# Kernel tuning notes

Hardware: AMD Instinct MI355X
Metric: run time of the kernel (lower is better)

Reference implementation:

```python
import jax, jax.numpy as jnp
import numpy as np

N_NODES = 100000
N_EDGES = 3200000
N_FEAT = 512
N_HID = 16
N_CLS = 7


def setup_inputs() -> dict:
    key = jax.random.key(0)
    k0, k1, k2, k3 = jax.random.split(key, 4)
    x = jax.random.normal(k0, (N_NODES, N_FEAT), dtype=jnp.float32)
    edge_index = jax.random.randint(k1, (2, N_EDGES), 0, N_NODES, dtype=jnp.int64)
    W1 = jax.random.normal(k2, (N_FEAT, N_HID), dtype=jnp.float32) * (1.0 / np.sqrt(N_FEAT))
    b1 = jnp.zeros((N_HID,), dtype=jnp.float32)
    W2 = jax.random.normal(k3, (N_HID, N_CLS), dtype=jnp.float32) * (1.0 / np.sqrt(N_HID))
    b2 = jnp.zeros((N_CLS,), dtype=jnp.float32)
    return {"x": x, "edge_index": edge_index, "W1": W1, "b1": b1, "W2": W2, "b2": b2}


def _graph_conv(x, src, dst, W, b, n_nodes):
    # transform-then-aggregate: keeps the gathered edge tensor at hidden width
    h = x @ W                                      # [N, out]
    agg = jax.ops.segment_sum(h[src], dst, num_segments=n_nodes)  # [N, out]
    return agg + b


def reference(x, edge_index, W1, b1, W2, b2):
    src, dst = edge_index[0], edge_index[1]
    h = jax.nn.relu(_graph_conv(x, src, dst, W1, b1, N_NODES))
    # dropout is identity in eval mode
    out = _graph_conv(h, src, dst, W2, b2, N_NODES)
    return jax.nn.log_softmax(out, axis=1)
```

## Files before the change

kernel.cpp:

```cpp
#include <hip/hip_runtime.h>

#define NN 100000
#define NE 3200000
#define NF 512
#define NH 16
#define NC 7

__global__ __launch_bounds__(256) void gemm1_kernel(const float* __restrict__ x,
                                                    const float* __restrict__ W1,
                                                    float* __restrict__ h0) {
  const int lane = threadIdx.x & 63;
  const int wave = (blockIdx.x * blockDim.x + threadIdx.x) >> 6;
  const int nwaves = (gridDim.x * blockDim.x) >> 6;

  float w[8][NH];
#pragma unroll
  for (int i = 0; i < 4; ++i) {
#pragma unroll
    for (int j = 0; j < NH; ++j) {
      w[i][j]     = W1[(4 * lane + i) * NH + j];
      w[4 + i][j] = W1[(256 + 4 * lane + i) * NH + j];
    }
  }

  for (int row = wave; row < NN; row += nwaves) {
    const float4* xr = (const float4*)(x + (size_t)row * NF);
    float4 a0 = xr[lane];
    float4 a1 = xr[64 + lane];
    float a[8] = {a0.x, a0.y, a0.z, a0.w, a1.x, a1.y, a1.z, a1.w};

    float acc[NH];
#pragma unroll
    for (int j = 0; j < NH; ++j) acc[j] = 0.f;
#pragma unroll
    for (int i = 0; i < 8; ++i) {
#pragma unroll
      for (int j = 0; j < NH; ++j) acc[j] += a[i] * w[i][j];
    }

    float outv = 0.f;
#pragma unroll
    for (int j = 0; j < NH; ++j) {
      float v = acc[j];
      v += __shfl_xor(v, 1);
      v += __shfl_xor(v, 2);
      v += __shfl_xor(v, 4);
      v += __shfl_xor(v, 8);
      v += __shfl_xor(v, 16);
      v += __shfl_xor(v, 32);
      if (lane == j) outv = v;
    }
    if (lane < NH) h0[(size_t)row * NH + lane] = outv;
  }
}

__global__ __launch_bounds__(256) void scatter16_kernel(const int* __restrict__ ei,
                                                        const float* __restrict__ h0,
                                                        float* __restrict__ agg) {
  long long gid = (long long)blockIdx.x * blockDim.x + threadIdx.x;
  int e = (int)(gid >> 4);
  if (e >= NE) return;
  int j = (int)(gid & 15);
  int s = ei[e];
  int d = ei[NE + e];
  atomicAdd(&agg[(size_t)d * NH + j], h0[(size_t)s * NH + j]);
}

__global__ __launch_bounds__(256) void transform_kernel(const float* __restrict__ agg1,
                                                        const float* __restrict__ b1,
                                                        const float* __restrict__ W2,
                                                        float* __restrict__ p) {
  int n = blockIdx.x * blockDim.x + threadIdx.x;
  if (n >= NN) return;
  const float4* r = (const float4*)(agg1 + (size_t)n * NH);
  float4 v0 = r[0], v1 = r[1], v2 = r[2], v3 = r[3];
  float h[NH] = {v0.x, v0.y, v0.z, v0.w, v1.x, v1.y, v1.z, v1.w,
                 v2.x, v2.y, v2.z, v2.w, v3.x, v3.y, v3.z, v3.w};
#pragma unroll
  for (int k = 0; k < NH; ++k) h[k] = fmaxf(h[k] + b1[k], 0.f);

#pragma unroll
  for (int j = 0; j < NC; ++j) {
    float acc = 0.f;
#pragma unroll
    for (int k = 0; k < NH; ++k) acc += h[k] * W2[k * NC + j];
    p[(size_t)n * 8 + j] = acc;
  }
}

__global__ __launch_bounds__(256) void scatter7_kernel(const int* __restrict__ ei,
                                                       const float* __restrict__ p,
                                                       float* __restrict__ agg) {
  long long gid = (long long)blockIdx.x * blockDim.x + threadIdx.x;
  int e = (int)(gid >> 3);
  if (e >= NE) return;
  int j = (int)(gid & 7);
  if (j >= NC) return;
  int s = ei[e];
  int d = ei[NE + e];
  atomicAdd(&agg[(size_t)d * 8 + j], p[(size_t)s * 8 + j]);
}

__global__ __launch_bounds__(256) void lsm_kernel(const float* __restrict__ agg2,
                                                  const float* __restrict__ b2,
                                                  float* __restrict__ out) {
  int n = blockIdx.x * blockDim.x + threadIdx.x;
  if (n >= NN) return;
  float z[NC];
  float m = -1e30f;
#pragma unroll
  for (int j = 0; j < NC; ++j) {
    z[j] = agg2[(size_t)n * 8 + j] + b2[j];
    m = fmaxf(m, z[j]);
  }
  float s = 0.f;
#pragma unroll
  for (int j = 0; j < NC; ++j) s += __expf(z[j] - m);
  float l = __logf(s);
#pragma unroll
  for (int j = 0; j < NC; ++j) out[(size_t)n * NC + j] = z[j] - m - l;
}

extern "C" void kernel_launch(void* const* d_in, const int* in_sizes, int n_in,
                              void* d_out, int out_size, void* d_ws, size_t ws_size,
                              hipStream_t stream) {
  const float* x  = (const float*)d_in[0];
  const int*   ei = (const int*)d_in[1];
  const float* W1 = (const float*)d_in[2];
  const float* b1 = (const float*)d_in[3];
  const float* W2 = (const float*)d_in[4];
  const float* b2 = (const float*)d_in[5];
  float* out = (float*)d_out;

  float* bufA = (float*)d_ws;
  float* bufB = bufA + (size_t)NN * NH;

  hipMemsetAsync(bufB, 0, (size_t)NN * NH * sizeof(float), stream);
  gemm1_kernel<<<2048, 256, 0, stream>>>(x, W1, bufA);
  scatter16_kernel<<<(int)(((long long)NE * 16 + 255) / 256), 256, 0, stream>>>(ei, bufA, bufB);
  transform_kernel<<<(NN + 255) / 256, 256, 0, stream>>>(bufB, b1, W2, bufA);
  hipMemsetAsync(bufB, 0, (size_t)NN * 8 * sizeof(float), stream);
  scatter7_kernel<<<(int)(((long long)NE * 8 + 255) / 256), 256, 0, stream>>>(ei, bufA, bufB);
  lsm_kernel<<<(NN + 255) / 256, 256, 0, stream>>>(bufB, b2, out);
}
```

Baseline: 704.9 us.

## Bucket edges by destination and aggregate in shared memory with fused epilogues

Edges are partitioned into buckets of 128 destination nodes using a histogram, a scan and a partition pass. Each agg kernel then accumulates one bucket in LDS, which replaces global float atomics, and fuses the bias/ReLU/W2 transform and the log-softmax into its epilogue. The GEMM now processes two rows per wave and uses a butterfly transpose-reduce instead of 16 separate full reductions. Sorting costs extra passes over the edge list plus a packed edge buffer, and the packing relies on node ids fitting in 17 bits.

```diff
diff --git a/kernel.cpp b/kernel.cpp
--- a/kernel.cpp
+++ b/kernel.cpp
@@ -6,119 +6,244 @@
 #define NH 16
 #define NC 7
 
+#define NBUCK 782
+#define PBLK 196
+#define EPT 64
+
+__device__ __forceinline__ float reduce16(const float acc[16], int lane) {
+  float w8[8];
+#pragma unroll
+  for (int i = 0; i < 8; ++i) {
+    float sel = (lane & 1) ? acc[2 * i + 1] : acc[2 * i];
+    float oth = (lane & 1) ? acc[2 * i]     : acc[2 * i + 1];
+    w8[i] = sel + __shfl_xor(oth, 1);
+  }
+  float w4[4];
+#pragma unroll
+  for (int i = 0; i < 4; ++i) {
+    float sel = (lane & 2) ? w8[2 * i + 1] : w8[2 * i];
+    float oth = (lane & 2) ? w8[2 * i]     : w8[2 * i + 1];
+    w4[i] = sel + __shfl_xor(oth, 2);
+  }
+  float w2[2];
+#pragma unroll
+  for (int i = 0; i < 2; ++i) {
+    float sel = (lane & 4) ? w4[2 * i + 1] : w4[2 * i];
+    float oth = (lane & 4) ? w4[2 * i]     : w4[2 * i + 1];
+    w2[i] = sel + __shfl_xor(oth, 4);
+  }
+  float sel = (lane & 8) ? w2[1] : w2[0];
+  float oth = (lane & 8) ? w2[0] : w2[1];
+  float v = sel + __shfl_xor(oth, 8);
+  v += __shfl_xor(v, 16);
+  v += __shfl_xor(v, 32);
+  return v;
+}
+
 __global__ __launch_bounds__(256) void gemm1_kernel(const float* __restrict__ x,
                                                     const float* __restrict__ W1,
                                                     float* __restrict__ h0) {
   const int lane = threadIdx.x & 63;
   const int wave = (blockIdx.x * blockDim.x + threadIdx.x) >> 6;
-  const int nwaves = (gridDim.x * blockDim.x) >> 6;
+  const int nw   = (gridDim.x * blockDim.x) >> 6;
 
   float w[8][NH];
 #pragma unroll
-  for (int i = 0; i < 4; ++i) {
+  for (int i = 0; i < 4; ++i)
 #pragma unroll
     for (int j = 0; j < NH; ++j) {
       w[i][j]     = W1[(4 * lane + i) * NH + j];
       w[4 + i][j] = W1[(256 + 4 * lane + i) * NH + j];
     }
-  }
-
-  for (int row = wave; row < NN; row += nwaves) {
-    const float4* xr = (const float4*)(x + (size_t)row * NF);
-    float4 a0 = xr[lane];
-    float4 a1 = xr[64 + lane];
-    float a[8] = {a0.x, a0.y, a0.z, a0.w, a1.x, a1.y, a1.z, a1.w};
-
-    float acc[NH];
-#pragma unroll
-    for (int j = 0; j < NH; ++j) acc[j] = 0.f;
-#pragma unroll
-    for (int i = 0; i < 8; ++i) {
-#pragma unroll
-      for (int j = 0; j < NH; ++j) acc[j] += a[i] * w[i][j];
-    }
-
-    float outv = 0.f;
-#pragma unroll
-    for (int j = 0; j < NH; ++j) {
-      float v = acc[j];
-      v += __shfl_xor(v, 1);
-      v += __shfl_xor(v, 2);
-      v += __shfl_xor(v, 4);
-      v += __shfl_xor(v, 8);
-      v += __shfl_xor(v, 16);
-      v += __shfl_xor(v, 32);
-      if (lane == j) outv = v;
-    }
-    if (lane < NH) h0[(size_t)row * NH + lane] = outv;
-  }
-}
-
-__global__ __launch_bounds__(256) void scatter16_kernel(const int* __restrict__ ei,
-                                                        const float* __restrict__ h0,
-                                                        float* __restrict__ agg) {
-  long long gid = (long long)blockIdx.x * blockDim.x + threadIdx.x;
-  int e = (int)(gid >> 4);
-  if (e >= NE) return;
-  int j = (int)(gid & 15);
-  int s = ei[e];
-  int d = ei[NE + e];
-  atomicAdd(&agg[(size_t)d * NH + j], h0[(size_t)s * NH + j]);
-}
-
-__global__ __launch_bounds__(256) void transform_kernel(const float* __restrict__ agg1,
-                                                        const float* __restrict__ b1,
-                                                        const float* __restrict__ W2,
-                                                        float* __restrict__ p) {
-  int n = blockIdx.x * blockDim.x + threadIdx.x;
-  if (n >= NN) return;
-  const float4* r = (const float4*)(agg1 + (size_t)n * NH);
-  float4 v0 = r[0], v1 = r[1], v2 = r[2], v3 = r[3];
-  float h[NH] = {v0.x, v0.y, v0.z, v0.w, v1.x, v1.y, v1.z, v1.w,
-                 v2.x, v2.y, v2.z, v2.w, v3.x, v3.y, v3.z, v3.w};
-#pragma unroll
-  for (int k = 0; k < NH; ++k) h[k] = fmaxf(h[k] + b1[k], 0.f);
-
-#pragma unroll
-  for (int j = 0; j < NC; ++j) {
-    float acc = 0.f;
-#pragma unroll
-    for (int k = 0; k < NH; ++k) acc += h[k] * W2[k * NC + j];
-    p[(size_t)n * 8 + j] = acc;
-  }
-}
-
-__global__ __launch_bounds__(256) void scatter7_kernel(const int* __restrict__ ei,
-                                                       const float* __restrict__ p,
-                                                       float* __restrict__ agg) {
-  long long gid = (long long)blockIdx.x * blockDim.x + threadIdx.x;
-  int e = (int)(gid >> 3);
-  if (e >= NE) return;
-  int j = (int)(gid & 7);
-  if (j >= NC) return;
-  int s = ei[e];
-  int d = ei[NE + e];
-  atomicAdd(&agg[(size_t)d * 8 + j], p[(size_t)s * 8 + j]);
-}
-
-__global__ __launch_bounds__(256) void lsm_kernel(const float* __restrict__ agg2,
-                                                  const float* __restrict__ b2,
-                                                  float* __restrict__ out) {
-  int n = blockIdx.x * blockDim.x + threadIdx.x;
-  if (n >= NN) return;
-  float z[NC];
-  float m = -1e30f;
-#pragma unroll
-  for (int j = 0; j < NC; ++j) {
-    z[j] = agg2[(size_t)n * 8 + j] + b2[j];
-    m = fmaxf(m, z[j]);
-  }
-  float s = 0.f;
-#pragma unroll
-  for (int j = 0; j < NC; ++j) s += __expf(z[j] - m);
-  float l = __logf(s);
-#pragma unroll
-  for (int j = 0; j < NC; ++j) out[(size_t)n * NC + j] = z[j] - m - l;
+
+  for (int pr = wave; pr < NN / 2; pr += nw) {
+    int r0 = 2 * pr;
+    const float4* x0 = (const float4*)(x + (size_t)r0 * NF);
+    const float4* x1 = (const float4*)(x + (size_t)(r0 + 1) * NF);
+    float4 a0 = x0[lane], b0 = x0[64 + lane];
+    float4 a1 = x1[lane], b1 = x1[64 + lane];
+    float A0[8] = {a0.x, a0.y, a0.z, a0.w, b0.x, b0.y, b0.z, b0.w};
+    float A1[8] = {a1.x, a1.y, a1.z, a1.w, b1.x, b1.y, b1.z, b1.w};
+    float c0[NH], c1[NH];
+#pragma unroll
+    for (int j = 0; j < NH; ++j) { c0[j] = 0.f; c1[j] = 0.f; }
+#pragma unroll
+    for (int i = 0; i < 8; ++i)
+#pragma unroll
+      for (int j = 0; j < NH; ++j) {
+        c0[j] += A0[i] * w[i][j];
+        c1[j] += A1[i] * w[i][j];
+      }
+    float v0 = reduce16(c0, lane);
+    float v1 = reduce16(c1, lane);
+    if (lane < 16)      h0[(size_t)r0 * NH + lane] = v0;
+    else if (lane < 32) h0[(size_t)(r0 + 1) * NH + (lane & 15)] = v1;
+  }
+}
+
+__global__ __launch_bounds__(256) void bucket_hist_kernel(const int* __restrict__ ei,
+                                                          int* __restrict__ gcount) {
+  __shared__ int hist[NBUCK];
+  for (int i = threadIdx.x; i < NBUCK; i += 256) hist[i] = 0;
+  __syncthreads();
+  int base = blockIdx.x * (256 * EPT);
+#pragma unroll 4
+  for (int it = 0; it < EPT; ++it) {
+    int e = base + it * 256 + threadIdx.x;
+    if (e < NE) atomicAdd(&hist[ei[NE + e] >> 7], 1);
+  }
+  __syncthreads();
+  for (int i = threadIdx.x; i < NBUCK; i += 256) {
+    int c = hist[i];
+    if (c) atomicAdd(&gcount[i], c);
+  }
+}
+
+__global__ __launch_bounds__(1024) void bucket_scan_kernel(const int* __restrict__ gcount,
+                                                           int* __restrict__ gbase,
+                                                           int* __restrict__ gcursor) {
+  __shared__ int tmp[1024];
+  int tid = threadIdx.x;
+  int v = (tid < NBUCK) ? gcount[tid] : 0;
+  tmp[tid] = v;
+  __syncthreads();
+  for (int off = 1; off < 1024; off <<= 1) {
+    int t = (tid >= off) ? tmp[tid - off] : 0;
+    __syncthreads();
+    tmp[tid] += t;
+    __syncthreads();
+  }
+  if (tid < NBUCK) {
+    int excl = tmp[tid] - v;
+    gbase[tid]   = excl;
+    gcursor[tid] = excl;
+  }
+  if (tid == 0) gbase[NBUCK] = NE;
+}
+
+__global__ __launch_bounds__(256) void partition_kernel(const int* __restrict__ ei,
+                                                        int* __restrict__ gcursor,
+                                                        int* __restrict__ ebuf) {
+  __shared__ int hist[NBUCK];
+  __shared__ int cbase[NBUCK];
+  for (int i = threadIdx.x; i < NBUCK; i += 256) hist[i] = 0;
+  __syncthreads();
+  int base = blockIdx.x * (256 * EPT);
+#pragma unroll 4
+  for (int it = 0; it < EPT; ++it) {
+    int e = base + it * 256 + threadIdx.x;
+    if (e < NE) atomicAdd(&hist[ei[NE + e] >> 7], 1);
+  }
+  __syncthreads();
+  for (int i = threadIdx.x; i < NBUCK; i += 256) {
+    int c = hist[i];
+    cbase[i] = c ? atomicAdd(&gcursor[i], c) : 0;
+  }
+  __syncthreads();
+  for (int i = threadIdx.x; i < NBUCK; i += 256) hist[i] = 0;
+  __syncthreads();
+#pragma unroll 4
+  for (int it = 0; it < EPT; ++it) {
+    int e = base + it * 256 + threadIdx.x;
+    if (e < NE) {
+      int d = ei[NE + e];
+      int s = ei[e];
+      int b = d >> 7;
+      int off = atomicAdd(&hist[b], 1);
+      ebuf[cbase[b] + off] = ((d & 127) << 17) | s;
+    }
+  }
+}
+
+__global__ __launch_bounds__(256) void agg1_kernel(const int* __restrict__ gbase,
+                                                   const int* __restrict__ ebuf,
+                                                   const float* __restrict__ h0,
+                                                   const float* __restrict__ b1,
+                                                   const float* __restrict__ W2,
+                                                   float* __restrict__ p) {
+  __shared__ float acc[128 * 17];
+  for (int i = threadIdx.x; i < 128 * 17; i += 256) acc[i] = 0.f;
+  __syncthreads();
+  int b = blockIdx.x;
+  int start = gbase[b], end = gbase[b + 1];
+  int eg = threadIdx.x >> 2, c = threadIdx.x & 3;
+  for (int e = start + eg; e < end; e += 64) {
+    int pk = ebuf[e];
+    int s  = pk & 0x1FFFF;
+    int li = pk >> 17;
+    float4 hv = *(const float4*)(h0 + (size_t)s * NH + 4 * c);
+    float* a = &acc[li * 17 + 4 * c];
+    atomicAdd(a + 0, hv.x);
+    atomicAdd(a + 1, hv.y);
+    atomicAdd(a + 2, hv.z);
+    atomicAdd(a + 3, hv.w);
+  }
+  __syncthreads();
+  int li = threadIdx.x;
+  if (li < 128) {
+    int node = (b << 7) + li;
+    if (node < NN) {
+      float h[NH];
+#pragma unroll
+      for (int k = 0; k < NH; ++k) h[k] = fmaxf(acc[li * 17 + k] + b1[k], 0.f);
+      float o[8];
+#pragma unroll
+      for (int j = 0; j < NC; ++j) {
+        float s = 0.f;
+#pragma unroll
+        for (int k = 0; k < NH; ++k) s += h[k] * W2[k * NC + j];
+        o[j] = s;
+      }
+      o[7] = 0.f;
+      float4* pr = (float4*)(p + (size_t)node * 8);
+      pr[0] = make_float4(o[0], o[1], o[2], o[3]);
+      pr[1] = make_float4(o[4], o[5], o[6], o[7]);
+    }
+  }
+}
+
+__global__ __launch_bounds__(256) void agg2_kernel(const int* __restrict__ gbase,
+                                                   const int* __restrict__ ebuf,
+                                                   const float* __restrict__ p,
+                                                   const float* __restrict__ b2,
+                                                   float* __restrict__ out) {
+  __shared__ float acc[128 * 9];
+  for (int i = threadIdx.x; i < 128 * 9; i += 256) acc[i] = 0.f;
+  __syncthreads();
+  int b = blockIdx.x;
+  int start = gbase[b], end = gbase[b + 1];
+  int eg = threadIdx.x >> 1, c = threadIdx.x & 1;
+  for (int e = start + eg; e < end; e += 128) {
+    int pk = ebuf[e];
+    int s  = pk & 0x1FFFF;
+    int li = pk >> 17;
+    float4 pv = *(const float4*)(p + (size_t)s * 8 + 4 * c);
+    float* a = &acc[li * 9 + 4 * c];
+    atomicAdd(a + 0, pv.x);
+    atomicAdd(a + 1, pv.y);
+    atomicAdd(a + 2, pv.z);
+    atomicAdd(a + 3, pv.w);
+  }
+  __syncthreads();
+  int li = threadIdx.x;
+  if (li < 128) {
+    int node = (b << 7) + li;
+    if (node < NN) {
+      float z[NC];
+      float m = -1e30f;
+#pragma unroll
+      for (int j = 0; j < NC; ++j) {
+        z[j] = acc[li * 9 + j] + b2[j];
+        m = fmaxf(m, z[j]);
+      }
+      float s = 0.f;
+#pragma unroll
+      for (int j = 0; j < NC; ++j) s += __expf(z[j] - m);
+      float l = __logf(s);
+#pragma unroll
+      for (int j = 0; j < NC; ++j) out[(size_t)node * NC + j] = z[j] - m - l;
+    }
+  }
 }
 
 extern "C" void kernel_launch(void* const* d_in, const int* in_sizes, int n_in,
@@ -132,14 +257,18 @@
   const float* b2 = (const float*)d_in[5];
   float* out = (float*)d_out;
 
-  float* bufA = (float*)d_ws;
-  float* bufB = bufA + (size_t)NN * NH;
-
-  hipMemsetAsync(bufB, 0, (size_t)NN * NH * sizeof(float), stream);
-  gemm1_kernel<<<2048, 256, 0, stream>>>(x, W1, bufA);
-  scatter16_kernel<<<(int)(((long long)NE * 16 + 255) / 256), 256, 0, stream>>>(ei, bufA, bufB);
-  transform_kernel<<<(NN + 255) / 256, 256, 0, stream>>>(bufB, b1, W2, bufA);
-  hipMemsetAsync(bufB, 0, (size_t)NN * 8 * sizeof(float), stream);
-  scatter7_kernel<<<(int)(((long long)NE * 8 + 255) / 256), 256, 0, stream>>>(ei, bufA, bufB);
-  lsm_kernel<<<(NN + 255) / 256, 256, 0, stream>>>(bufB, b2, out);
-}
+  float* h0      = (float*)d_ws;
+  float* p       = h0 + (size_t)NN * NH;
+  int*   ebuf    = (int*)(p + (size_t)NN * 8);
+  int*   gcount  = ebuf + NE;
+  int*   gbase   = gcount + NBUCK;
+  int*   gcursor = gbase + NBUCK + 1;
+
+  hipMemsetAsync(gcount, 0, NBUCK * sizeof(int), stream);
+  bucket_hist_kernel<<<PBLK, 256, 0, stream>>>(ei, gcount);
+  bucket_scan_kernel<<<1, 1024, 0, stream>>>(gcount, gbase, gcursor);
+  partition_kernel<<<PBLK, 256, 0, stream>>>(ei, gcursor, ebuf);
+  gemm1_kernel<<<2048, 256, 0, stream>>>(x, W1, h0);
+  agg1_kernel<<<NBUCK, 256, 0, stream>>>(gbase, ebuf, h0, b1, W2, p);
+  agg2_kernel<<<NBUCK, 256, 0, stream>>>(gbase, ebuf, p, b2, out);
+}
```

Result: slower. 916.9 us (+30.1%).
